# Kernel tuning notes

Measured on AMD Instinct MI355X. Metric: run time of the kernel, lower is better.

## Reference

```python
import jax, jax.numpy as jnp
import numpy as np

M = 150000  # number of nodes
K = 64      # neighbor_limits[-1]


def setup_inputs() -> dict:
    key = jax.random.key(0)
    k1, k2 = jax.random.split(key)
    nodes = jax.random.normal(k1, (M, 3), dtype=jnp.float32)
    # radius_search-style neighbor table: values in [0, M], where index == M is padding
    node_knn_indices = jax.random.randint(k2, (M, K), 0, M + 1, dtype=jnp.int64)
    return {"nodes": nodes, "node_knn_indices": node_knn_indices}


def _greedy_nms(knn):
    # Sequential greedy suppression: node i is kept iff none of its radius
    # neighbors with smaller index was already kept. masks has size M+1 so the
    # padding index M always reads False (never suppresses).
    m = knn.shape[0]
    masks0 = jnp.zeros(m + 1, dtype=bool)

    def step(masks, xs):
        i, row = xs
        keep = ~jnp.any(masks[row])  # masks[node_knn_indices[i]].sum() == 0
        return masks.at[i].set(keep), None

    masks, _ = jax.lax.scan(step, masks0, (jnp.arange(m), knn))
    return masks


def reference(nodes, node_knn_indices):
    masks = _greedy_nms(node_knn_indices)
    kept = masks[:-1]  # [M] bool
    # Original returns node_knn_indices[kept] (data-dependent shape). For a
    # jit-compatible fixed shape we return the full table with suppressed rows
    # overwritten by the padding index M; kept rows are bitwise identical.
    m = node_knn_indices.shape[0]
    kept_knn = jnp.where(kept[:, None], node_knn_indices, m)
    return kept, kept_knn
```

## Files before the change

### kernel.cpp

```cpp
#include <hip/hip_runtime.h>


#define M_ROWS 150000
#define KNN    64
#define BLK    1024
#define QRT    2
#define CHUNK  (BLK * QRT)
#define NCH    ((M_ROWS + CHUNK - 1) / CHUNK)
#define ICAP   6
#define ECAP   24
#define WCH    16
#define W64PC  (CHUNK / 32)
#define LMW    (((NCH - 1) * CHUNK) / 32)
#define NBMG   ((NCH - 1) * W64PC)
#define OUT_INTS (M_ROWS + M_ROWS * KNN)
#define BMG_INT_OFF (OUT_INTS - NBMG * 2)
#define DECFULL 0xffffffffu

__global__ void init_ws_kernel(unsigned int* done, int* out) {
  const int i = blockIdx.x * blockDim.x + threadIdx.x;
  unsigned long long* bmg64 = (unsigned long long*)(out + BMG_INT_OFF);
  if (i < NBMG) bmg64[i] = 0ull;
  if (i == 0) *done = 0u;
}

__device__ __forceinline__ bool probe_reload(const int* __restrict__ rp,
                                             const unsigned int* lm,
                                             int lo, int hi) {
  bool s = false;
#pragma unroll
  for (int u = 0; u < 16; ++u) {
    int4 d = ((const int4*)rp)[u];
    int js[4] = {d.x, d.y, d.z, d.w};
#pragma unroll
    for (int m = 0; m < 4; ++m) {
      int j = js[m];
      if (j >= lo && j < hi && ((lm[j >> 5] >> (j & 31)) & 1u)) s = true;
    }
  }
  return s;
}

__global__ __launch_bounds__(BLK) void nms_chain_kernel(
    const int* __restrict__ knn,
    int* __restrict__ out,
    unsigned int* __restrict__ done)
{
  const int b    = blockIdx.x;
  const int t    = threadIdx.x;
  const int base = b * CHUNK;
  const int winb = (b > WCH) ? (base - WCH * CHUNK) : 0;

  unsigned long long* bmg64 = (unsigned long long*)(out + BMG_INT_OFF);

  __shared__ unsigned char      st[CHUNK];
  __shared__ unsigned short     il[ICAP][CHUNK];
  __shared__ unsigned short     exl[ECAP][CHUNK];
  __shared__ unsigned int       lm[LMW];
  __shared__ unsigned int       sh_p;

  int  rowq[QRT];
  bool vq[QRT], ovf[QRT], eovf[QRT], supp[QRT];
  int  ic[QRT], ec[QRT];

#pragma unroll
  for (int q = 0; q < QRT; ++q) {
    rowq[q] = base + q * BLK + t;
    vq[q]   = rowq[q] < M_ROWS;
    ic[q] = ec[q] = 0;
    ovf[q] = eovf[q] = supp[q] = false;
  }

#pragma unroll
  for (int q = 0; q < QRT; ++q) {
    if (!vq[q]) continue;
    const int o   = q * BLK + t;
    const int row = rowq[q];
    const int* rp = knn + (long long)row * KNN;
#pragma unroll
    for (int u = 0; u < 16; ++u) {
      int4 d = ((const int4*)rp)[u];
      int js[4] = {d.x, d.y, d.z, d.w};
#pragma unroll
      for (int m = 0; m < 4; ++m) {
        int j = js[m];
        if (j < row) {
          if (j >= base) {
            if (ic[q] < ICAP) il[ic[q]][o] = (unsigned short)(j - base);
            ++ic[q];
          } else if (j >= winb) {
            if (ec[q] < ECAP) exl[ec[q]][o] = (unsigned short)(j - winb);
            ++ec[q];
          }
        }
      }
    }
  }
#pragma unroll
  for (int q = 0; q < QRT; ++q) {
    ovf[q]  = ic[q] > ICAP; if (ovf[q])  ic[q] = ICAP;
    eovf[q] = ec[q] > ECAP; if (eovf[q]) ec[q] = ECAP;
  }

  unsigned short ilr[QRT][ICAP];
#pragma unroll
  for (int q = 0; q < QRT; ++q)
#pragma unroll
    for (int x = 0; x < ICAP; ++x)
      ilr[q][x] = il[x][q * BLK + t];

  int praw1 = 0;
  if (b > WCH) {
    if (t < 64) {
      int pr = 0;
      for (int spin = 0; spin < (1 << 22); ++spin) {
        pr = (int)__hip_atomic_load(done, __ATOMIC_RELAXED,
                                    __HIP_MEMORY_SCOPE_AGENT);
        if (pr >= b - WCH) break;
        __builtin_amdgcn_s_sleep(2);
      }
      if (t == 0) sh_p = (unsigned int)pr;
    }
    __syncthreads();
    praw1 = (int)sh_p; if (praw1 > b) praw1 = b;
    const int wt = praw1 * W64PC;
    for (int w = t; w < wt; w += BLK) {
      unsigned long long v = __hip_atomic_load(&bmg64[w], __ATOMIC_RELAXED,
                                               __HIP_MEMORY_SCOPE_AGENT);
      int g1 = 0;
      while (((unsigned int)(v >> 32)) != DECFULL && ++g1 < (1 << 22)) {
        __builtin_amdgcn_s_sleep(1);
        v = __hip_atomic_load(&bmg64[w], __ATOMIC_RELAXED,
                              __HIP_MEMORY_SCOPE_AGENT);
      }
      lm[w] = (unsigned int)v;
    }
    __syncthreads();
    const int lim = praw1 * CHUNK;
#pragma unroll
    for (int q = 0; q < QRT; ++q)
      if (vq[q])
        supp[q] = probe_reload(knn + (long long)rowq[q] * KNN, lm, 0, lim);
  }
  const int pr1lim = praw1 * CHUNK;

  unsigned int extm[QRT];
  bool eunk[QRT];
#pragma unroll
  for (int q = 0; q < QRT; ++q) {
    extm[q] = 0u; eunk[q] = false;
    if (vq[q] && !supp[q]) {
      const int o = q * BLK + t;
      const int n = ec[q];
#pragma unroll
      for (int x = 0; x < ECAP; ++x) {
        if (x < n) {
          const int j = winb + (int)exl[x][o];
          if (j >= pr1lim) extm[q] |= (1u << x);
        }
      }
      eunk[q] = eovf[q];
    }
  }

  unsigned char myst[QRT];
#pragma unroll
  for (int q = 0; q < QRT; ++q) {
    myst[q] = (!vq[q] || supp[q]) ? (unsigned char)2
            : ((ic[q] == 0 && !ovf[q] && extm[q] == 0u && !eunk[q])
               ? (unsigned char)1 : (unsigned char)0);
    __hip_atomic_store(&st[q * BLK + t], myst[q],
                       __ATOMIC_RELAXED, __HIP_MEMORY_SCOPE_WORKGROUP);
  }
  __syncthreads();

  const int lane = t & 63;
  const bool pub = (b < NCH - 1);
  if (pub) {
#pragma unroll
    for (int q = 0; q < QRT; ++q) {
      unsigned long long bdec  = __ballot(myst[q] != 0);
      unsigned long long bkept = __ballot(myst[q] == 1);
      const int g = b * W64PC + ((q * BLK + (t & ~63)) >> 5);
      if (lane == 0)
        (void)__hip_atomic_fetch_or(&bmg64[g],
            ((bdec & 0xffffffffull) << 32) | (bkept & 0xffffffffull),
            __ATOMIC_RELAXED, __HIP_MEMORY_SCOPE_AGENT);
      if (lane == 32)
        (void)__hip_atomic_fetch_or(&bmg64[g + 1],
            ((bdec >> 32) << 32) | (bkept >> 32),
            __ATOMIC_RELAXED, __HIP_MEMORY_SCOPE_AGENT);
    }
  }

  bool undec = false;
#pragma unroll
  for (int q = 0; q < QRT; ++q) undec |= (myst[q] == 0);

  for (int pass = 0; pass < (1 << 22); ++pass) {
    bool pend = false;
    if (undec) {
#pragma unroll
      for (int q = 0; q < QRT; ++q) {
        if (myst[q] != 0) continue;
        const int o   = q * BLK + t;
        const int row = base + o;
        bool anyK = false, allD = true;
        unsigned int m = extm[q];

        if (m != 0u) {
#pragma unroll
          for (int g = 0; g < 3; ++g) {
            if ((m >> (g * 8)) & 0xffu) {
              unsigned long long vv[8];
#pragma unroll
              for (int x = 0; x < 8; ++x) {
                const int xe = g * 8 + x;
                const int j = winb + (int)exl[xe][o];
                const int w = ((m >> xe) & 1u) ? (j >> 5) : 0;
                vv[x] = __hip_atomic_load(&bmg64[w], __ATOMIC_RELAXED,
                                          __HIP_MEMORY_SCOPE_AGENT);
              }
#pragma unroll
              for (int x = 0; x < 8; ++x) {
                const int xe = g * 8 + x;
                if ((m >> xe) & 1u) {
                  const int j = winb + (int)exl[xe][o];
                  const int bit = j & 31;
                  if ((((unsigned int)(vv[x] >> 32)) >> bit) & 1u) {
                    if ((((unsigned int)vv[x]) >> bit) & 1u) anyK = true;
                    m &= ~(1u << xe);
                  } else pend = true;
                }
              }
            }
          }
          extm[q] = m;
        }

        if (!ovf[q]) {
          unsigned char vsts[ICAP];
#pragma unroll
          for (int x = 0; x < ICAP; ++x) {
            const int ii = (x < ic[q]) ? (int)ilr[q][x] : 0;
            vsts[x] = __hip_atomic_load(&st[ii],
                __ATOMIC_RELAXED, __HIP_MEMORY_SCOPE_WORKGROUP);
          }
#pragma unroll
          for (int x = 0; x < ICAP; ++x) {
            if (x < ic[q]) { anyK |= (vsts[x] == 1); allD &= (vsts[x] != 0); }
          }
        } else {
          const int* rp = knn + (long long)row * KNN;
#pragma unroll
          for (int u = 0; u < 16; ++u) {
            int4 d = ((const int4*)rp)[u];
            int js[4] = {d.x, d.y, d.z, d.w};
            unsigned char sv[4];
#pragma unroll
            for (int m2 = 0; m2 < 4; ++m2) {
              const bool in = (js[m2] >= base && js[m2] < row);
              sv[m2] = __hip_atomic_load(&st[in ? (js[m2] - base) : 0],
                  __ATOMIC_RELAXED, __HIP_MEMORY_SCOPE_WORKGROUP);
            }
#pragma unroll
            for (int m2 = 0; m2 < 4; ++m2) {
              if (js[m2] >= base && js[m2] < row) {
                anyK |= (sv[m2] == 1); allD &= (sv[m2] != 0);
              }
            }
          }
        }
        if (extm[q] != 0u) allD = false;

        if (!anyK && eunk[q]) {
          const int lo = (pr1lim > winb) ? pr1lim : winb;
          const int* rp = knn + (long long)row * KNN;
          bool ep = false, ak = false;
#pragma unroll
          for (int g = 0; g < 8; ++g) {
            int js[8];
#pragma unroll
            for (int u = 0; u < 2; ++u) {
              int4 d = ((const int4*)rp)[g * 2 + u];
              js[u * 4 + 0] = d.x; js[u * 4 + 1] = d.y;
              js[u * 4 + 2] = d.z; js[u * 4 + 3] = d.w;
            }
            unsigned long long wv[8];
#pragma unroll
            for (int m2 = 0; m2 < 8; ++m2) {
              const bool in = (js[m2] >= lo && js[m2] < base);
              wv[m2] = __hip_atomic_load(&bmg64[in ? (js[m2] >> 5) : 0],
                  __ATOMIC_RELAXED, __HIP_MEMORY_SCOPE_AGENT);
            }
#pragma unroll
            for (int m2 = 0; m2 < 8; ++m2) {
              if (js[m2] >= lo && js[m2] < base) {
                const int bit = js[m2] & 31;
                if ((((unsigned int)(wv[m2] >> 32)) >> bit) & 1u) {
                  if ((((unsigned int)wv[m2]) >> bit) & 1u) ak = true;
                } else ep = true;
              }
            }
          }
          if (ak) anyK = true;
          else if (!ep) eunk[q] = false;
          if (ep) pend = true;
        }
        if (eunk[q]) allD = false;

        if (anyK)      myst[q] = 2;
        else if (allD) myst[q] = 1;
        if (myst[q] != 0) {
          __hip_atomic_store(&st[o], myst[q],
                             __ATOMIC_RELAXED, __HIP_MEMORY_SCOPE_WORKGROUP);
          if (pub) {
            const int g = b * W64PC + (o >> 5);
            const int bit = o & 31;
            unsigned long long val = (1ull << (32 + bit))
                | ((myst[q] == 1) ? (1ull << bit) : 0ull);
            (void)__hip_atomic_fetch_or(&bmg64[g], val,
                __ATOMIC_RELAXED, __HIP_MEMORY_SCOPE_AGENT);
          }
        }
      }

#pragma unroll
      for (int s = 0; s < 2; ++s) {
#pragma unroll
        for (int q = 0; q < QRT; ++q) {
          if (myst[q] != 0 || ovf[q]) continue;
          const int o = q * BLK + t;
          bool anyK = false, allD = true;
          unsigned char vsts[ICAP];
#pragma unroll
          for (int x = 0; x < ICAP; ++x) {
            const int ii = (x < ic[q]) ? (int)ilr[q][x] : 0;
            vsts[x] = __hip_atomic_load(&st[ii],
                __ATOMIC_RELAXED, __HIP_MEMORY_SCOPE_WORKGROUP);
          }
#pragma unroll
          for (int x = 0; x < ICAP; ++x) {
            if (x < ic[q]) { anyK |= (vsts[x] == 1); allD &= (vsts[x] != 0); }
          }
          if (extm[q] != 0u || eunk[q]) allD = false;
          if (anyK)      myst[q] = 2;
          else if (allD) myst[q] = 1;
          if (myst[q] != 0) {
            __hip_atomic_store(&st[o], myst[q],
                               __ATOMIC_RELAXED, __HIP_MEMORY_SCOPE_WORKGROUP);
            if (pub) {
              const int g = b * W64PC + (o >> 5);
              const int bit = o & 31;
              unsigned long long val = (1ull << (32 + bit))
                  | ((myst[q] == 1) ? (1ull << bit) : 0ull);
              (void)__hip_atomic_fetch_or(&bmg64[g], val,
                  __ATOMIC_RELAXED, __HIP_MEMORY_SCOPE_AGENT);
            }
          }
        }
      }

      undec = false;
#pragma unroll
      for (int q = 0; q < QRT; ++q) undec |= (myst[q] == 0);
    }

    if (__ballot(undec) == 0ull) break;
    if (__ballot(pend) != 0ull) __builtin_amdgcn_s_sleep(1);
  }

  __syncthreads();
  if (pub) {
#pragma unroll
    for (int q = 0; q < QRT; ++q) {
      unsigned long long bkept = __ballot(myst[q] == 1);
      const int g = b * W64PC + ((q * BLK + (t & ~63)) >> 5);
      if (lane == 0)
        __hip_atomic_store(&bmg64[g],
            (0xffffffffull << 32) | (bkept & 0xffffffffull),
            __ATOMIC_RELAXED, __HIP_MEMORY_SCOPE_AGENT);
      if (lane == 32)
        __hip_atomic_store(&bmg64[g + 1],
            (0xffffffffull << 32) | (bkept >> 32),
            __ATOMIC_RELAXED, __HIP_MEMORY_SCOPE_AGENT);
    }
  }
  __syncthreads();
  if (pub && t == 0)
    (void)__hip_atomic_fetch_add(done, 1u,
        __ATOMIC_RELEASE, __HIP_MEMORY_SCOPE_AGENT);

  if (b == NCH - 1) {
    if (t < 64) {
      for (int spin = 0; spin < (1 << 22); ++spin) {
        unsigned int dv = __hip_atomic_load(done, __ATOMIC_ACQUIRE,
                                            __HIP_MEMORY_SCOPE_AGENT);
        if (dv >= (unsigned int)(NCH - 1)) break;
        __builtin_amdgcn_s_sleep(2);
      }
    }
    __syncthreads();
  }

  bool kq[QRT];
#pragma unroll
  for (int q = 0; q < QRT; ++q)
    kq[q] = vq[q] && (myst[q] == 1);

#pragma unroll
  for (int q = 0; q < QRT; ++q)
    if (vq[q]) out[rowq[q]] = kq[q] ? 1 : 0;

#pragma unroll
  for (int q = 0; q < QRT; ++q) {
    if (!vq[q]) continue;
    const int row = rowq[q];
    const int* rp = knn + (long long)row * KNN;
    int* orow = out + M_ROWS + (long long)row * KNN;
    const bool k = kq[q];
#pragma unroll
    for (int u = 0; u < 16; ++u) {
      int4 d = ((const int4*)rp)[u];
      int4 o4;
      o4.x = k ? d.x : M_ROWS;
      o4.y = k ? d.y : M_ROWS;
      o4.z = k ? d.z : M_ROWS;
      o4.w = k ? d.w : M_ROWS;
      ((int4*)orow)[u] = o4;
    }
  }
}

extern "C" void kernel_launch(void* const* d_in, const int* in_sizes, int n_in,
                              void* d_out, int out_size, void* d_ws, size_t ws_size,
                              hipStream_t stream) {
  const int* knn = (const int*)d_in[1];
  int* out = (int*)d_out;
  unsigned int* done = (unsigned int*)d_ws;

  init_ws_kernel<<<(NBMG + BLK - 1) / BLK, BLK, 0, stream>>>(done, out);
  nms_chain_kernel<<<NCH, BLK, 0, stream>>>(knn, out, done);
}
```

Before: 364.2 us.

## Replace window shared-bitmap reload with direct global bitmap probe of earlier neighbors

Removes the shared-memory copy of the whole decided bitmap prefix and the 16-chunk window external neighbor list. Each row now probes the global decided/kept bitmap directly for every neighbor in earlier chunks, and keeps up to 12 still-undecided neighbor indices in registers, falling back to a full rescan on overflow. The throttle wait now only ensures the block runs at most 12 chunks ahead. This drops a large shared array and its serial reload but adds scattered global atomic loads per neighbor and more register pressure.

```diff
diff --git a/kernel.cpp b/kernel.cpp
--- a/kernel.cpp
+++ b/kernel.cpp
@@ -8,37 +8,18 @@
 #define CHUNK  (BLK * QRT)
 #define NCH    ((M_ROWS + CHUNK - 1) / CHUNK)
 #define ICAP   6
-#define ECAP   24
-#define WCH    16
+#define UCAP   12
+#define THRB   12
 #define W64PC  (CHUNK / 32)
-#define LMW    (((NCH - 1) * CHUNK) / 32)
 #define NBMG   ((NCH - 1) * W64PC)
 #define OUT_INTS (M_ROWS + M_ROWS * KNN)
 #define BMG_INT_OFF (OUT_INTS - NBMG * 2)
-#define DECFULL 0xffffffffu
 
 __global__ void init_ws_kernel(unsigned int* done, int* out) {
   const int i = blockIdx.x * blockDim.x + threadIdx.x;
   unsigned long long* bmg64 = (unsigned long long*)(out + BMG_INT_OFF);
   if (i < NBMG) bmg64[i] = 0ull;
   if (i == 0) *done = 0u;
-}
-
-__device__ __forceinline__ bool probe_reload(const int* __restrict__ rp,
-                                             const unsigned int* lm,
-                                             int lo, int hi) {
-  bool s = false;
-#pragma unroll
-  for (int u = 0; u < 16; ++u) {
-    int4 d = ((const int4*)rp)[u];
-    int js[4] = {d.x, d.y, d.z, d.w};
-#pragma unroll
-    for (int m = 0; m < 4; ++m) {
-      int j = js[m];
-      if (j >= lo && j < hi && ((lm[j >> 5] >> (j & 31)) & 1u)) s = true;
-    }
-  }
-  return s;
 }
 
 __global__ __launch_bounds__(BLK) void nms_chain_kernel(
@@ -49,26 +30,26 @@
   const int b    = blockIdx.x;
   const int t    = threadIdx.x;
   const int base = b * CHUNK;
-  const int winb = (b > WCH) ? (base - WCH * CHUNK) : 0;
 
   unsigned long long* bmg64 = (unsigned long long*)(out + BMG_INT_OFF);
 
-  __shared__ unsigned char      st[CHUNK];
-  __shared__ unsigned short     il[ICAP][CHUNK];
-  __shared__ unsigned short     exl[ECAP][CHUNK];
-  __shared__ unsigned int       lm[LMW];
-  __shared__ unsigned int       sh_p;
+  __shared__ unsigned char  st[CHUNK];
+  __shared__ unsigned short il[ICAP][CHUNK];
 
   int  rowq[QRT];
-  bool vq[QRT], ovf[QRT], eovf[QRT], supp[QRT];
-  int  ic[QRT], ec[QRT];
+  bool vq[QRT], ovf[QRT], supp[QRT], oflow[QRT];
+  int  ic[QRT];
+  int  uj[QRT][UCAP];
+  unsigned int um[QRT];
 
 #pragma unroll
   for (int q = 0; q < QRT; ++q) {
     rowq[q] = base + q * BLK + t;
     vq[q]   = rowq[q] < M_ROWS;
-    ic[q] = ec[q] = 0;
-    ovf[q] = eovf[q] = supp[q] = false;
+    ic[q] = 0; um[q] = 0u;
+    ovf[q] = supp[q] = oflow[q] = false;
+#pragma unroll
+    for (int x = 0; x < UCAP; ++x) uj[q][x] = 0;
   }
 
 #pragma unroll
@@ -84,22 +65,16 @@
 #pragma unroll
       for (int m = 0; m < 4; ++m) {
         int j = js[m];
-        if (j < row) {
-          if (j >= base) {
-            if (ic[q] < ICAP) il[ic[q]][o] = (unsigned short)(j - base);
-            ++ic[q];
-          } else if (j >= winb) {
-            if (ec[q] < ECAP) exl[ec[q]][o] = (unsigned short)(j - winb);
-            ++ec[q];
-          }
-        }
-      }
-    }
-  }
-#pragma unroll
-  for (int q = 0; q < QRT; ++q) {
-    ovf[q]  = ic[q] > ICAP; if (ovf[q])  ic[q] = ICAP;
-    eovf[q] = ec[q] > ECAP; if (eovf[q]) ec[q] = ECAP;
+        if (j >= base && j < row) {
+          if (ic[q] < ICAP) il[ic[q]][o] = (unsigned short)(j - base);
+          ++ic[q];
+        }
+      }
+    }
+  }
+#pragma unroll
+  for (int q = 0; q < QRT; ++q) {
+    ovf[q] = ic[q] > ICAP; if (ovf[q]) ic[q] = ICAP;
   }
 
   unsigned short ilr[QRT][ICAP];
@@ -109,65 +84,63 @@
     for (int x = 0; x < ICAP; ++x)
       ilr[q][x] = il[x][q * BLK + t];
 
-  int praw1 = 0;
-  if (b > WCH) {
+  if (b > THRB) {
     if (t < 64) {
-      int pr = 0;
       for (int spin = 0; spin < (1 << 22); ++spin) {
-        pr = (int)__hip_atomic_load(done, __ATOMIC_RELAXED,
-                                    __HIP_MEMORY_SCOPE_AGENT);
-        if (pr >= b - WCH) break;
-        __builtin_amdgcn_s_sleep(2);
-      }
-      if (t == 0) sh_p = (unsigned int)pr;
+        unsigned int pr = __hip_atomic_load(done, __ATOMIC_RELAXED,
+                                            __HIP_MEMORY_SCOPE_AGENT);
+        if ((int)pr >= b - THRB) break;
+        __builtin_amdgcn_s_sleep(8);
+      }
     }
     __syncthreads();
-    praw1 = (int)sh_p; if (praw1 > b) praw1 = b;
-    const int wt = praw1 * W64PC;
-    for (int w = t; w < wt; w += BLK) {
-      unsigned long long v = __hip_atomic_load(&bmg64[w], __ATOMIC_RELAXED,
-                                               __HIP_MEMORY_SCOPE_AGENT);
-      int g1 = 0;
-      while (((unsigned int)(v >> 32)) != DECFULL && ++g1 < (1 << 22)) {
-        __builtin_amdgcn_s_sleep(1);
-        v = __hip_atomic_load(&bmg64[w], __ATOMIC_RELAXED,
-                              __HIP_MEMORY_SCOPE_AGENT);
-      }
-      lm[w] = (unsigned int)v;
-    }
-    __syncthreads();
-    const int lim = praw1 * CHUNK;
-#pragma unroll
-    for (int q = 0; q < QRT; ++q)
-      if (vq[q])
-        supp[q] = probe_reload(knn + (long long)rowq[q] * KNN, lm, 0, lim);
-  }
-  const int pr1lim = praw1 * CHUNK;
-
-  unsigned int extm[QRT];
-  bool eunk[QRT];
-#pragma unroll
-  for (int q = 0; q < QRT; ++q) {
-    extm[q] = 0u; eunk[q] = false;
-    if (vq[q] && !supp[q]) {
-      const int o = q * BLK + t;
-      const int n = ec[q];
-#pragma unroll
-      for (int x = 0; x < ECAP; ++x) {
-        if (x < n) {
-          const int j = winb + (int)exl[x][o];
-          if (j >= pr1lim) extm[q] |= (1u << x);
-        }
-      }
-      eunk[q] = eovf[q];
-    }
+  }
+
+#pragma unroll
+  for (int q = 0; q < QRT; ++q) {
+    if (!vq[q] || b == 0) continue;
+    const int row = rowq[q];
+    const int* rp = knn + (long long)row * KNN;
+    bool anyK0 = false;
+    int uc = 0;
+#pragma unroll
+    for (int g = 0; g < 8; ++g) {
+      int4 d0 = ((const int4*)rp)[g * 2];
+      int4 d1 = ((const int4*)rp)[g * 2 + 1];
+      int js[8] = {d0.x, d0.y, d0.z, d0.w, d1.x, d1.y, d1.z, d1.w};
+      unsigned long long wv[8];
+#pragma unroll
+      for (int m2 = 0; m2 < 8; ++m2) {
+        const bool in = js[m2] < base;
+        wv[m2] = __hip_atomic_load(&bmg64[in ? (js[m2] >> 5) : 0],
+            __ATOMIC_RELAXED, __HIP_MEMORY_SCOPE_AGENT);
+      }
+#pragma unroll
+      for (int m2 = 0; m2 < 8; ++m2) {
+        if (js[m2] < base) {
+          const int bit = js[m2] & 31;
+          if ((((unsigned int)(wv[m2] >> 32)) >> bit) & 1u) {
+            if ((((unsigned int)wv[m2]) >> bit) & 1u) anyK0 = true;
+          } else {
+            if (uc < UCAP) {
+#pragma unroll
+              for (int x = 0; x < UCAP; ++x)
+                if (uc == x) uj[q][x] = js[m2];
+              ++uc;
+            } else oflow[q] = true;
+          }
+        }
+      }
+    }
+    supp[q] = anyK0;
+    um[q] = oflow[q] ? 0u : ((1u << uc) - 1u);
   }
 
   unsigned char myst[QRT];
 #pragma unroll
   for (int q = 0; q < QRT; ++q) {
     myst[q] = (!vq[q] || supp[q]) ? (unsigned char)2
-            : ((ic[q] == 0 && !ovf[q] && extm[q] == 0u && !eunk[q])
+            : ((ic[q] == 0 && !ovf[q] && um[q] == 0u && !oflow[q])
                ? (unsigned char)1 : (unsigned char)0);
     __hip_atomic_store(&st[q * BLK + t], myst[q],
                        __ATOMIC_RELAXED, __HIP_MEMORY_SCOPE_WORKGROUP);
@@ -206,37 +179,53 @@
         const int o   = q * BLK + t;
         const int row = base + o;
         bool anyK = false, allD = true;
-        unsigned int m = extm[q];
-
-        if (m != 0u) {
-#pragma unroll
-          for (int g = 0; g < 3; ++g) {
-            if ((m >> (g * 8)) & 0xffu) {
-              unsigned long long vv[8];
-#pragma unroll
-              for (int x = 0; x < 8; ++x) {
-                const int xe = g * 8 + x;
-                const int j = winb + (int)exl[xe][o];
-                const int w = ((m >> xe) & 1u) ? (j >> 5) : 0;
-                vv[x] = __hip_atomic_load(&bmg64[w], __ATOMIC_RELAXED,
-                                          __HIP_MEMORY_SCOPE_AGENT);
-              }
-#pragma unroll
-              for (int x = 0; x < 8; ++x) {
-                const int xe = g * 8 + x;
-                if ((m >> xe) & 1u) {
-                  const int j = winb + (int)exl[xe][o];
-                  const int bit = j & 31;
-                  if ((((unsigned int)(vv[x] >> 32)) >> bit) & 1u) {
-                    if ((((unsigned int)vv[x]) >> bit) & 1u) anyK = true;
-                    m &= ~(1u << xe);
-                  } else pend = true;
-                }
-              }
-            }
-          }
-          extm[q] = m;
-        }
+        unsigned int m = um[q];
+
+        if (m & 0xffu) {
+          unsigned long long vv[8];
+#pragma unroll
+          for (int x = 0; x < 8; ++x) {
+            const int j = uj[q][x];
+            const int w = ((m >> x) & 1u) ? (j >> 5) : 0;
+            vv[x] = __hip_atomic_load(&bmg64[w], __ATOMIC_RELAXED,
+                                      __HIP_MEMORY_SCOPE_AGENT);
+          }
+#pragma unroll
+          for (int x = 0; x < 8; ++x) {
+            if ((m >> x) & 1u) {
+              const int j = uj[q][x];
+              const int bit = j & 31;
+              if ((((unsigned int)(vv[x] >> 32)) >> bit) & 1u) {
+                if ((((unsigned int)vv[x]) >> bit) & 1u) anyK = true;
+                m &= ~(1u << x);
+              } else pend = true;
+            }
+          }
+        }
+        if (m >> 8) {
+          unsigned long long vv[4];
+#pragma unroll
+          for (int x = 0; x < 4; ++x) {
+            const int xe = 8 + x;
+            const int j = uj[q][xe];
+            const int w = ((m >> xe) & 1u) ? (j >> 5) : 0;
+            vv[x] = __hip_atomic_load(&bmg64[w], __ATOMIC_RELAXED,
+                                      __HIP_MEMORY_SCOPE_AGENT);
+          }
+#pragma unroll
+          for (int x = 0; x < 4; ++x) {
+            const int xe = 8 + x;
+            if ((m >> xe) & 1u) {
+              const int j = uj[q][xe];
+              const int bit = j & 31;
+              if ((((unsigned int)(vv[x] >> 32)) >> bit) & 1u) {
+                if ((((unsigned int)vv[x]) >> bit) & 1u) anyK = true;
+                m &= ~(1u << xe);
+              } else pend = true;
+            }
+          }
+        }
+        um[q] = m;
 
         if (!ovf[q]) {
           unsigned char vsts[ICAP];
@@ -271,31 +260,26 @@
             }
           }
         }
-        if (extm[q] != 0u) allD = false;
-
-        if (!anyK && eunk[q]) {
-          const int lo = (pr1lim > winb) ? pr1lim : winb;
+        if (um[q] != 0u) allD = false;
+
+        if (!anyK && oflow[q]) {
           const int* rp = knn + (long long)row * KNN;
           bool ep = false, ak = false;
 #pragma unroll
           for (int g = 0; g < 8; ++g) {
-            int js[8];
-#pragma unroll
-            for (int u = 0; u < 2; ++u) {
-              int4 d = ((const int4*)rp)[g * 2 + u];
-              js[u * 4 + 0] = d.x; js[u * 4 + 1] = d.y;
-              js[u * 4 + 2] = d.z; js[u * 4 + 3] = d.w;
-            }
+            int4 d0 = ((const int4*)rp)[g * 2];
+            int4 d1 = ((const int4*)rp)[g * 2 + 1];
+            int js[8] = {d0.x, d0.y, d0.z, d0.w, d1.x, d1.y, d1.z, d1.w};
             unsigned long long wv[8];
 #pragma unroll
             for (int m2 = 0; m2 < 8; ++m2) {
-              const bool in = (js[m2] >= lo && js[m2] < base);
+              const bool in = js[m2] < base;
               wv[m2] = __hip_atomic_load(&bmg64[in ? (js[m2] >> 5) : 0],
                   __ATOMIC_RELAXED, __HIP_MEMORY_SCOPE_AGENT);
             }
 #pragma unroll
             for (int m2 = 0; m2 < 8; ++m2) {
-              if (js[m2] >= lo && js[m2] < base) {
+              if (js[m2] < base) {
                 const int bit = js[m2] & 31;
                 if ((((unsigned int)(wv[m2] >> 32)) >> bit) & 1u) {
                   if ((((unsigned int)wv[m2]) >> bit) & 1u) ak = true;
@@ -304,10 +288,10 @@
             }
           }
           if (ak) anyK = true;
-          else if (!ep) eunk[q] = false;
+          else if (!ep) oflow[q] = false;
           if (ep) pend = true;
         }
-        if (eunk[q]) allD = false;
+        if (oflow[q]) allD = false;
 
         if (anyK)      myst[q] = 2;
         else if (allD) myst[q] = 1;
@@ -343,7 +327,7 @@
           for (int x = 0; x < ICAP; ++x) {
             if (x < ic[q]) { anyK |= (vsts[x] == 1); allD &= (vsts[x] != 0); }
           }
-          if (extm[q] != 0u || eunk[q]) allD = false;
+          if (um[q] != 0u || oflow[q]) allD = false;
           if (anyK)      myst[q] = 2;
           else if (allD) myst[q] = 1;
           if (myst[q] != 0) {
```

New measurement: 727.5 us. +99.8%, slower.
